# Performance work log

Measured on AMD Instinct MI355X. Metric: run time of the kernel, lower is better.

The kernel has to match this reference:

```python
import jax, jax.numpy as jnp
import numpy as np

LAMB = 0.01
DISTILL = 1.0
NUM_CLASSES = 10


def _reverse_seq(x, lens):
    # TF reverse_sequence semantics: reverse first `lens[i]` steps of row i.
    T = x.shape[1]
    t = jnp.arange(T)[None, :]
    idx = jnp.where(t < lens[:, None], lens[:, None] - 1 - t, t)
    return jnp.take_along_axis(x, idx[:, :, None], axis=1)


def _run_gru(x, lens, Wg, bg, Wc, bc):
    # TF GRUCell: r,z = sigmoid([x,h]Wg + bg); c = tanh([x, r*h]Wc + bc); h' = z*h + (1-z)*c
    # dynamic_rnn: past sequence_length, state is frozen and output is zero.
    N, T, _ = x.shape
    H = Wc.shape[1]
    h0 = jnp.zeros((N, H), x.dtype)

    def step(h, inp):
        x_t, t = inp
        xh = jnp.concatenate([x_t, h], axis=-1)
        rz = jax.nn.sigmoid(xh @ Wg + bg)
        r, z = jnp.split(rz, 2, axis=-1)
        c = jnp.tanh(jnp.concatenate([x_t, r * h], axis=-1) @ Wc + bc)
        h_new = z * h + (1.0 - z) * c
        valid = (t < lens)[:, None]
        return jnp.where(valid, h_new, h), jnp.where(valid, h_new, 0.0)

    _, outs = jax.lax.scan(step, h0, (x.transpose(1, 0, 2), jnp.arange(T)))
    return outs.transpose(1, 0, 2)  # [N, T, H]


def _bigru(x, lens, pfw, pbw):
    fw = _run_gru(x, lens, *pfw)
    bw = _reverse_seq(_run_gru(_reverse_seq(x, lens), lens, *pbw), lens)
    return jnp.concatenate([fw, bw], axis=-1)  # [N, T, 2H]


def _attention(out, Wa, ba, u):
    # additive attention: tanh projection -> score with context vector -> softmax -> weighted sum
    proj = jnp.tanh(out @ Wa + ba)                      # [N, T, A]
    score = jnp.squeeze(proj @ u, -1) / DISTILL         # [N, T]
    att = jax.nn.softmax(score, axis=1)
    vec = jnp.einsum('nt,nth->nh', att, out)            # [N, 2H]
    return vec, att


def setup_inputs() -> dict:
    key = jax.random.key(0)
    ks = jax.random.split(key, 40)
    B, D, S, E, H, C = 64, 40, 50, 200, 128, 10
    rn = lambda k, shp, s=0.1: (jax.random.normal(k, shp) * s).astype(jnp.float32)
    inp = {}
    inp['X_sentence'] = jax.random.normal(ks[0], (B, D, S, E), jnp.float32)
    inp['y'] = jax.random.randint(ks[1], (B,), 0, C).astype(jnp.int32)
    inp['sentence_length'] = jax.random.randint(ks[2], (B * D,), 1, S + 1).astype(jnp.int32)
    inp['document_length'] = jax.random.randint(ks[3], (B,), 1, D + 1).astype(jnp.int32)
    inp['dropout'] = 0
    inp['is_training'] = 0
    i = [4]
    def nxt():
        k = ks[i[0]]; i[0] += 1; return k
    for lvl, din in (('l', E), ('h', 2 * H)):
        for d in ('f', 'b'):
            inp['wg' + d + '_' + lvl] = rn(nxt(), (din + H, 2 * H))
            inp['bg' + d + '_' + lvl] = jnp.ones((2 * H,), jnp.float32)  # TF GRU gate bias init = 1.0
            inp['wc' + d + '_' + lvl] = rn(nxt(), (din + H, H))
            inp['bc' + d + '_' + lvl] = jnp.zeros((H,), jnp.float32)
        inp['wa_' + lvl] = rn(nxt(), (2 * H, H))
        inp['ba_' + lvl] = jnp.zeros((H,), jnp.float32)
    inp['uw'] = rn(nxt(), (H, 1), 1.0)  # random_normal stddev=1.0 as in source
    inp['us'] = rn(nxt(), (H, 1), 1.0)
    inp['wp'] = rn(nxt(), (2 * H, C))
    inp['bp'] = jnp.zeros((C,), jnp.float32)
    return inp


def reference(X_sentence, y, sentence_length, document_length, dropout, is_training,
              wgf_l, bgf_l, wcf_l, bcf_l, wgb_l, bgb_l, wcb_l, bcb_l, wa_l, ba_l,
              wgf_h, bgf_h, wcf_h, bcf_h, wgb_h, bgb_h, wcb_h, bcb_h, wa_h, ba_h,
              uw, us, wp, bp):
    # inference mode (is_training=False -> tf.layers.dropout is identity)
    B, D, S, E = X_sentence.shape
    x = X_sentence.reshape(B * D, S, E)
    # word level
    low = _bigru(x, sentence_length, (wgf_l, bgf_l, wcf_l, bcf_l), (wgb_l, bgb_l, wcb_l, bcb_l))
    sent_vec, att_low = _attention(low, wa_l, ba_l, uw)            # [B*D, 2H], [B*D, S]
    sent = sent_vec.reshape(B, D, -1)
    # sentence level
    high = _bigru(sent, document_length, (wgf_h, bgf_h, wcf_h, bcf_h), (wgb_h, bgb_h, wcb_h, bcb_h))
    doc_vec, att_high = _attention(high, wa_h, ba_h, us)           # [B, 2H], [B, D]
    logits = doc_vec @ wp + bp                                     # [B, C]
    logp = jax.nn.log_softmax(logits, axis=-1)
    loss = -jnp.mean(jnp.take_along_axis(logp, y[:, None], axis=1))
    # regularizer exactly as in source (note h kernel counted twice, h bias omitted)
    loss = loss + LAMB * (jnp.sum(wa_l ** 2) + jnp.sum(ba_l ** 2)
                          + 2.0 * jnp.sum(wa_h ** 2)
                          + jnp.sum(uw ** 2) + jnp.sum(us ** 2))
    predict = jnp.argmax(logits, axis=1).astype(jnp.int32)
    accuracy = jnp.mean((y == predict).astype(jnp.float32))
    return (loss, predict, accuracy, att_low, att_high)
```

## Files before the change

kernel.cpp:

```cpp
#include <hip/hip_runtime.h>
#include <hip/hip_bf16.h>


typedef __attribute__((ext_vector_type(8))) short short8;
typedef __attribute__((ext_vector_type(4))) float f32x4;

__device__ __forceinline__ float fsigmoid(float x) { return 1.f / (1.f + __expf(-x)); }
__device__ __forceinline__ float ftanh(float x)    { float e = __expf(2.f * x); return 1.f - 2.f / (e + 1.f); }

__device__ __forceinline__ unsigned short f2bf(float x) {
    unsigned int u = __builtin_bit_cast(unsigned int, x);
    u += 0x7fffu + ((u >> 16) & 1u);
    return (unsigned short)(u >> 16);
}
__device__ __forceinline__ float bf2f(unsigned short h) {
    unsigned int u = ((unsigned int)h) << 16;
    return __builtin_bit_cast(float, u);
}
__device__ __forceinline__ uint4 pack8(const unsigned short* v) {
    uint4 r;
    r.x = (unsigned int)v[0] | ((unsigned int)v[1] << 16);
    r.y = (unsigned int)v[2] | ((unsigned int)v[3] << 16);
    r.z = (unsigned int)v[4] | ((unsigned int)v[5] << 16);
    r.w = (unsigned int)v[6] | ((unsigned int)v[7] << 16);
    return r;
}
__device__ __forceinline__ void cvt8(const float* v, short8& hi, short8& lo) {
    unsigned short h[8], l[8];
#pragma unroll
    for (int j = 0; j < 8; ++j) {
        unsigned short hh = f2bf(v[j]);
        h[j] = hh;
        l[j] = f2bf(v[j] - bf2f(hh));
    }
    uint4 uh = pack8(h), ul = pack8(l);
    hi = __builtin_bit_cast(short8, uh);
    lo = __builtin_bit_cast(short8, ul);
}

__global__ __launch_bounds__(256) void pack_weights(
    const float* __restrict__ wg_f, const float* __restrict__ bg_f,
    const float* __restrict__ wc_f, const float* __restrict__ bc_f,
    const float* __restrict__ wg_b, const float* __restrict__ bg_b,
    const float* __restrict__ wc_b, const float* __restrict__ bc_b,
    float* __restrict__ W, float* __restrict__ bias, int E)
{
    int idx = blockIdx.x * 256 + threadIdx.x;
    if (idx < 768) {
        int c = idx; float v;
        if (c < 256) v = bg_f[c];
        else if (c < 384) v = bc_f[c - 256];
        else if (c < 640) v = bg_b[c - 384];
        else v = bc_b[c - 640];
        bias[c] = v;
    }
    if (idx >= E * 768) return;
    int k = idx / 768, c = idx - k * 768;
    float v;
    if (c < 256) v = wg_f[k * 256 + c];
    else if (c < 384) v = wc_f[k * 128 + (c - 256)];
    else if (c < 640) v = wg_b[k * 256 + (c - 384)];
    else v = wc_b[k * 128 + (c - 640)];
    W[idx] = v;
}

__global__ __launch_bounds__(256) void pack_a_frag(
    const float* __restrict__ src, uint4* __restrict__ dstH, uint4* __restrict__ dstL,
    int Mr16, int KC, int Ks)
{
    int idx = blockIdx.x * 256 + threadIdx.x;
    if (idx >= Mr16 * KC * 64) return;
    int lane = idx & 63;
    int g = idx >> 6;
    int mb = g / KC, kc = g - mb * KC;
    int m = lane & 15, quad = lane >> 4;
    int row = mb * 16 + m;
    int k0 = kc * 32 + quad * 8;
    const float* s = src + (size_t)row * Ks;
    unsigned short hi[8], lo[8];
#pragma unroll
    for (int j = 0; j < 8; ++j) {
        float x = (k0 + j < Ks) ? s[k0 + j] : 0.f;
        unsigned short h = f2bf(x);
        hi[j] = h;
        lo[j] = f2bf(x - bf2f(h));
    }
    dstH[idx] = pack8(hi);
    dstL[idx] = pack8(lo);
}

__global__ __launch_bounds__(256) void pack_w_frag(
    const float* __restrict__ src, uint4* __restrict__ dstH, uint4* __restrict__ dstL,
    int N16, int KC, int Ks, int N)
{
    int idx = blockIdx.x * 256 + threadIdx.x;
    if (idx >= N16 * KC * 64) return;
    int lane = idx & 63;
    int g = idx >> 6;
    int nb = g / KC, kc = g - nb * KC;
    int m = lane & 15, quad = lane >> 4;
    int n = nb * 16 + m;
    int k0 = kc * 32 + quad * 8;
    unsigned short hi[8], lo[8];
#pragma unroll
    for (int j = 0; j < 8; ++j) {
        float x = (k0 + j < Ks) ? src[(size_t)(k0 + j) * N + n] : 0.f;
        unsigned short h = f2bf(x);
        hi[j] = h;
        lo[j] = f2bf(x - bf2f(h));
    }
    dstH[idx] = pack8(hi);
    dstL[idx] = pack8(lo);
}

__global__ __launch_bounds__(256) void mfma_gemm(
    const uint4* __restrict__ Ah, const uint4* __restrict__ Al,
    const uint4* __restrict__ Bh, const uint4* __restrict__ Bl,
    const float* __restrict__ bias, float* __restrict__ C,
    int KC, int ldc, int act)
{
    int tid = threadIdx.x;
    int lane = tid & 63;
    int w = tid >> 6;
    int wm = w >> 1, wn = w & 1;
    int quad = lane >> 4, m = lane & 15;
    int bm = blockIdx.x, bn = blockIdx.y;
    f32x4 acc[4][4];
#pragma unroll
    for (int i = 0; i < 4; ++i)
#pragma unroll
        for (int j = 0; j < 4; ++j) acc[i][j] = (f32x4){0.f, 0.f, 0.f, 0.f};

    size_t aBase[4], bBase[4];
#pragma unroll
    for (int i = 0; i < 4; ++i) {
        aBase[i] = ((size_t)(bm * 8 + wm * 4 + i) * KC) * 64 + quad * 16 + m;
        bBase[i] = ((size_t)(bn * 8 + wn * 4 + i) * KC) * 64 + quad * 16 + m;
    }
    for (int kc = 0; kc < KC; ++kc) {
        short8 ah[4], al[4], bh[4], bl[4];
#pragma unroll
        for (int i = 0; i < 4; ++i) {
            ah[i] = __builtin_bit_cast(short8, Ah[aBase[i]]);
            al[i] = __builtin_bit_cast(short8, Al[aBase[i]]);
            bh[i] = __builtin_bit_cast(short8, Bh[bBase[i]]);
            bl[i] = __builtin_bit_cast(short8, Bl[bBase[i]]);
            aBase[i] += 64; bBase[i] += 64;
        }
#pragma unroll
        for (int i = 0; i < 4; ++i)
#pragma unroll
            for (int j = 0; j < 4; ++j) {
                acc[i][j] = __builtin_amdgcn_mfma_f32_16x16x32_bf16(ah[i], bh[j], acc[i][j], 0, 0, 0);
                acc[i][j] = __builtin_amdgcn_mfma_f32_16x16x32_bf16(ah[i], bl[j], acc[i][j], 0, 0, 0);
                acc[i][j] = __builtin_amdgcn_mfma_f32_16x16x32_bf16(al[i], bh[j], acc[i][j], 0, 0, 0);
            }
    }
#pragma unroll
    for (int i = 0; i < 4; ++i) {
        int row0 = bm * 128 + wm * 64 + i * 16 + quad * 4;
#pragma unroll
        for (int j = 0; j < 4; ++j) {
            int col = bn * 128 + wn * 64 + j * 16 + m;
            float b = bias[col];
#pragma unroll
            for (int r = 0; r < 4; ++r) {
                float v = acc[i][j][r] + b;
                if (act) v = ftanh(v);
                C[(size_t)(row0 + r) * ldc + col] = v;
            }
        }
    }
}

__global__ __launch_bounds__(256) void bigru_mfma(
    const float* __restrict__ G,
    const uint4* __restrict__ WgH, const uint4* __restrict__ WgL,
    const uint4* __restrict__ WcH, const uint4* __restrict__ WcL,
    const int* __restrict__ lens,
    float* __restrict__ outbuf,
    int rowOff, int T)
{
    __shared__ float hs[16][132];
    __shared__ float rs_[16][132];
    __shared__ float zs[16][132];
    __shared__ int Ls[16];

    int tid = threadIdx.x;
    int dir = blockIdx.x & 1;
    int rg0 = (blockIdx.x >> 1) * 16;
    int lane = tid & 63, w = tid >> 6;
    int quad = lane >> 4, mc = lane & 15;
    for (int i = tid; i < 16 * 132; i += 256) (&hs[0][0])[i] = 0.f;
    if (tid < 16) Ls[tid] = lens[rowOff + rg0 + tid];
    __syncthreads();
    const int goff = dir * 384;

    for (int t = 0; t < T; ++t) {
        int Lr[4], tir[4];
#pragma unroll
        for (int r = 0; r < 4; ++r) {
            int L = Ls[quad * 4 + r];
            Lr[r] = L;
            tir[r] = dir ? ((t < L) ? (L - 1 - t) : t) : t;
        }
        float gG[4][4], gC[2][4];
#pragma unroll
        for (int r = 0; r < 4; ++r) {
            const float* gbase = &G[((size_t)(rg0 + quad * 4 + r) * T + tir[r]) * 768 + goff];
#pragma unroll
            for (int i = 0; i < 4; ++i) gG[i][r] = gbase[(w * 4 + i) * 16 + mc];
#pragma unroll
            for (int i = 0; i < 2; ++i) gC[i][r] = gbase[256 + (w * 2 + i) * 16 + mc];
        }
        short8 ahh[4], ahl[4];
#pragma unroll
        for (int kc = 0; kc < 4; ++kc) {
            float v[8];
            const float* hp = &hs[mc][kc * 32 + quad * 8];
#pragma unroll
            for (int j = 0; j < 8; ++j) v[j] = hp[j];
            cvt8(v, ahh[kc], ahl[kc]);
        }
        f32x4 ga[4];
#pragma unroll
        for (int i = 0; i < 4; ++i) ga[i] = (f32x4){0.f, 0.f, 0.f, 0.f};
#pragma unroll
        for (int kc = 0; kc < 4; ++kc) {
#pragma unroll
            for (int i = 0; i < 4; ++i) {
                size_t idx = (((size_t)(dir * 16 + w * 4 + i) * 4 + kc) << 6) + lane;
                short8 bh = __builtin_bit_cast(short8, WgH[idx]);
                short8 bl = __builtin_bit_cast(short8, WgL[idx]);
                ga[i] = __builtin_amdgcn_mfma_f32_16x16x32_bf16(ahh[kc], bh, ga[i], 0, 0, 0);
                ga[i] = __builtin_amdgcn_mfma_f32_16x16x32_bf16(ahh[kc], bl, ga[i], 0, 0, 0);
                ga[i] = __builtin_amdgcn_mfma_f32_16x16x32_bf16(ahl[kc], bh, ga[i], 0, 0, 0);
            }
        }
#pragma unroll
        for (int i = 0; i < 4; ++i) {
            int n = (w * 4 + i) * 16 + mc;
#pragma unroll
            for (int r = 0; r < 4; ++r) {
                int m = quad * 4 + r;
                float s = fsigmoid(ga[i][r] + gG[i][r]);
                if (n < 128) rs_[m][n] = s * hs[m][n];
                else zs[m][n - 128] = s;
            }
        }
        __syncthreads();
        short8 arh[4], arl[4];
#pragma unroll
        for (int kc = 0; kc < 4; ++kc) {
            float v[8];
            const float* rp = &rs_[mc][kc * 32 + quad * 8];
#pragma unroll
            for (int j = 0; j < 8; ++j) v[j] = rp[j];
            cvt8(v, arh[kc], arl[kc]);
        }
        f32x4 ca[2];
#pragma unroll
        for (int i = 0; i < 2; ++i) ca[i] = (f32x4){0.f, 0.f, 0.f, 0.f};
#pragma unroll
        for (int kc = 0; kc < 4; ++kc) {
#pragma unroll
            for (int i = 0; i < 2; ++i) {
                size_t idx = (((size_t)(dir * 8 + w * 2 + i) * 4 + kc) << 6) + lane;
                short8 bh = __builtin_bit_cast(short8, WcH[idx]);
                short8 bl = __builtin_bit_cast(short8, WcL[idx]);
                ca[i] = __builtin_amdgcn_mfma_f32_16x16x32_bf16(arh[kc], bh, ca[i], 0, 0, 0);
                ca[i] = __builtin_amdgcn_mfma_f32_16x16x32_bf16(arh[kc], bl, ca[i], 0, 0, 0);
                ca[i] = __builtin_amdgcn_mfma_f32_16x16x32_bf16(arl[kc], bh, ca[i], 0, 0, 0);
            }
        }
#pragma unroll
        for (int i = 0; i < 2; ++i) {
            int n = (w * 2 + i) * 16 + mc;
#pragma unroll
            for (int r = 0; r < 4; ++r) {
                int m = quad * 4 + r;
                bool valid = (t < Lr[r]);
                float cd = ftanh(ca[i][r] + gC[i][r]);
                float z = zs[m][n];
                float h = hs[m][n];
                float hn = z * h + (1.f - z) * cd;
                float ov = valid ? hn : 0.f;
                if (valid) hs[m][n] = hn;
                outbuf[((size_t)(rg0 + m) * T + tir[r]) * 256 + dir * 128 + n] = ov;
            }
        }
        __syncthreads();
    }
}

__global__ __launch_bounds__(64) void attn_reduce(
    const float* __restrict__ proj, const float* __restrict__ outv,
    const float* __restrict__ u,
    float* __restrict__ att_out, float* __restrict__ vec,
    int T, int attRowOff)
{
    int n = blockIdx.x, lane = threadIdx.x;
    float s = 0.f;
    if (lane < T) {
        const float4* p = (const float4*)(proj + ((size_t)n * T + lane) * 128);
        const float4* uu = (const float4*)u;
        for (int k = 0; k < 32; ++k) {
            float4 a = p[k], b = uu[k];
            s += a.x * b.x + a.y * b.y + a.z * b.z + a.w * b.w;
        }
    }
    float m = (lane < T) ? s : -3.402823466e38f;
    for (int o = 32; o > 0; o >>= 1) m = fmaxf(m, __shfl_xor(m, o));
    float e = (lane < T) ? __expf(s - m) : 0.f;
    float sum = e;
    for (int o = 32; o > 0; o >>= 1) sum += __shfl_xor(sum, o);
    float att = e / sum;
    if (lane < T) att_out[(size_t)(attRowOff + n) * T + lane] = att;
    float4 acc = {0.f, 0.f, 0.f, 0.f};
    for (int t = 0; t < T; ++t) {
        float a = __shfl(att, t);
        float4 o4 = *(const float4*)&outv[((size_t)n * T + t) * 256 + lane * 4];
        acc.x += a * o4.x; acc.y += a * o4.y; acc.z += a * o4.z; acc.w += a * o4.w;
    }
    *(float4*)&vec[(size_t)n * 256 + lane * 4] = acc;
}

__global__ __launch_bounds__(256) void head_kernel(
    const float* __restrict__ dvec, const float* __restrict__ wp, const float* __restrict__ bp,
    const int* __restrict__ y,
    const float* __restrict__ wa_l, const float* __restrict__ ba_l, const float* __restrict__ wa_h,
    const float* __restrict__ uw, const float* __restrict__ us,
    float* __restrict__ out)
{
    __shared__ float lg[64][10];
    __shared__ float red[256];
    int tid = threadIdx.x;
    for (int idx = tid; idx < 640; idx += 256) {
        int r = idx / 10, c = idx % 10;
        float a = bp[c];
        const float* dv = dvec + r * 256;
        for (int k = 0; k < 256; ++k) a += dv[k] * wp[k * 10 + c];
        lg[r][c] = a;
    }
    __syncthreads();
    float lossv = 0.f, corr = 0.f;
    if (tid < 64) {
        float m = lg[tid][0]; int arg = 0;
        for (int c = 1; c < 10; ++c) if (lg[tid][c] > m) { m = lg[tid][c]; arg = c; }
        float se = 0.f;
        for (int c = 0; c < 10; ++c) se += __expf(lg[tid][c] - m);
        float lse = m + __logf(se);
        int yy = y[tid];
        lossv = -(lg[tid][yy] - lse);
        corr = (yy == arg) ? 1.f : 0.f;
        out[1 + tid] = (float)arg;
    }
    float rs = 0.f;
    for (int i = tid; i < 32768; i += 256) {
        float v = wa_l[i]; rs += v * v;
        float w = wa_h[i]; rs += 2.f * w * w;
    }
    if (tid < 128) {
        float v1 = ba_l[tid], v2 = uw[tid], v3 = us[tid];
        rs += v1 * v1 + v2 * v2 + v3 * v3;
    }
    red[tid] = lossv; __syncthreads();
    for (int o = 128; o > 0; o >>= 1) { if (tid < o) red[tid] += red[tid + o]; __syncthreads(); }
    float totLoss = red[0]; __syncthreads();
    red[tid] = corr; __syncthreads();
    for (int o = 128; o > 0; o >>= 1) { if (tid < o) red[tid] += red[tid + o]; __syncthreads(); }
    float totCorr = red[0]; __syncthreads();
    red[tid] = rs; __syncthreads();
    for (int o = 128; o > 0; o >>= 1) { if (tid < o) red[tid] += red[tid + o]; __syncthreads(); }
    float totReg = red[0];
    if (tid == 0) {
        out[0] = totLoss / 64.f + 0.01f * totReg;
        out[65] = totCorr / 64.f;
    }
}

extern "C" void kernel_launch(void* const* d_in, const int* in_sizes, int n_in,
                              void* d_out, int out_size, void* d_ws, size_t ws_size,
                              hipStream_t stream)
{
    const float* X    = (const float*)d_in[0];
    const int*   y    = (const int*)d_in[1];
    const int*   slen = (const int*)d_in[2];
    const int*   dlen = (const int*)d_in[3];
    const float* wgf_l = (const float*)d_in[6];
    const float* bgf_l = (const float*)d_in[7];
    const float* wcf_l = (const float*)d_in[8];
    const float* bcf_l = (const float*)d_in[9];
    const float* wgb_l = (const float*)d_in[10];
    const float* bgb_l = (const float*)d_in[11];
    const float* wcb_l = (const float*)d_in[12];
    const float* bcb_l = (const float*)d_in[13];
    const float* wa_l  = (const float*)d_in[14];
    const float* ba_l  = (const float*)d_in[15];
    const float* wgf_h = (const float*)d_in[16];
    const float* bgf_h = (const float*)d_in[17];
    const float* wcf_h = (const float*)d_in[18];
    const float* bcf_h = (const float*)d_in[19];
    const float* wgb_h = (const float*)d_in[20];
    const float* bgb_h = (const float*)d_in[21];
    const float* wcb_h = (const float*)d_in[22];
    const float* bcb_h = (const float*)d_in[23];
    const float* wa_h  = (const float*)d_in[24];
    const float* ba_h  = (const float*)d_in[25];
    const float* uw    = (const float*)d_in[26];
    const float* us    = (const float*)d_in[27];
    const float* wp    = (const float*)d_in[28];
    const float* bp    = (const float*)d_in[29];
    float* out = (float*)d_out;

    int NCH = 1;
    while (NCH < 8) {
        size_t M1t = 128000ull / NCH;
        size_t needB = (M1t * 1248ull + 6000000ull) * 4ull;
        if (needB <= ws_size) break;
        NCH *= 2;
    }
    size_t nRows = 2560 / NCH;
    size_t M1 = nRows * 50;

    float* G1     = (float*)d_ws;
    float* low    = G1 + M1 * 768;
    float* AXf    = low + M1 * 256;
    float* sent   = AXf + M1 * 224;
    float* Gs     = sent + 655360;
    float* high   = Gs + 1966080;
    float* projs  = high + 655360;
    float* dvec   = projs + 327680;
    float* pSf    = dvec + 16384;
    float* pHf    = pSf + 655360;
    float* WpackL = pHf + 655360;
    float* biasL  = WpackL + 153600;
    float* WLf    = biasL + 768;
    float* WpackH = WLf + 172032;
    float* biasH  = WpackH + 196608;
    float* WHf    = biasH + 768;
    float* WaLf   = WHf + 196608;
    float* WaHf   = WaLf + 32768;
    float* RgLf   = WaHf + 32768;
    float* RcLf   = RgLf + 65536;
    float* RgHf   = RcLf + 32768;
    float* RcHf   = RgHf + 65536;

    uint4* AXh = (uint4*)AXf;           uint4* AXl = (uint4*)(AXf + M1 * 112);
    uint4* ALh = (uint4*)G1;            uint4* ALl = (uint4*)(G1 + M1 * 128);
    float* proj = G1 + M1 * 256;
    uint4* pSh = (uint4*)pSf;           uint4* pSl = (uint4*)(pSf + 327680);
    uint4* pHh = (uint4*)pHf;           uint4* pHl = (uint4*)(pHf + 327680);
    uint4* WLh = (uint4*)WLf;           uint4* WLl = (uint4*)(WLf + 86016);
    uint4* WHh = (uint4*)WHf;           uint4* WHl = (uint4*)(WHf + 98304);
    uint4* WaLh = (uint4*)WaLf;         uint4* WaLl = (uint4*)(WaLf + 16384);
    uint4* WaHh = (uint4*)WaHf;         uint4* WaHl = (uint4*)(WaHf + 16384);
    uint4* RgLH = (uint4*)RgLf;         uint4* RgLL = (uint4*)(RgLf + 32768);
    uint4* RcLH = (uint4*)RcLf;         uint4* RcLL = (uint4*)(RcLf + 16384);
    uint4* RgHH = (uint4*)RgHf;         uint4* RgHL = (uint4*)(RgHf + 32768);
    uint4* RcHH = (uint4*)RcHf;         uint4* RcHL = (uint4*)(RcHf + 16384);

    pack_weights<<<600, 256, 0, stream>>>(wgf_l, bgf_l, wcf_l, bcf_l, wgb_l, bgb_l, wcb_l, bcb_l,
                                          WpackL, biasL, 200);
    pack_weights<<<768, 256, 0, stream>>>(wgf_h, bgf_h, wcf_h, bcf_h, wgb_h, bgb_h, wcb_h, bcb_h,
                                          WpackH, biasH, 256);
    pack_w_frag<<<84, 256, 0, stream>>>(WpackL, WLh, WLl, 48, 7, 200, 768);
    pack_w_frag<<<96, 256, 0, stream>>>(WpackH, WHh, WHl, 48, 8, 256, 768);
    pack_w_frag<<<16, 256, 0, stream>>>(wa_l, WaLh, WaLl, 8, 8, 256, 128);
    pack_w_frag<<<16, 256, 0, stream>>>(wa_h, WaHh, WaHl, 8, 8, 256, 128);
    pack_w_frag<<<16, 256, 0, stream>>>(wgf_l + 200 * 256, RgLH,        RgLL,        16, 4, 128, 256);
    pack_w_frag<<<16, 256, 0, stream>>>(wgb_l + 200 * 256, RgLH + 4096, RgLL + 4096, 16, 4, 128, 256);
    pack_w_frag<<< 8, 256, 0, stream>>>(wcf_l + 200 * 128, RcLH,        RcLL,         8, 4, 128, 128);
    pack_w_frag<<< 8, 256, 0, stream>>>(wcb_l + 200 * 128, RcLH + 2048, RcLL + 2048,  8, 4, 128, 128);
    pack_w_frag<<<16, 256, 0, stream>>>(wgf_h + 256 * 256, RgHH,        RgHL,        16, 4, 128, 256);
    pack_w_frag<<<16, 256, 0, stream>>>(wgb_h + 256 * 256, RgHH + 4096, RgHL + 4096, 16, 4, 128, 256);
    pack_w_frag<<< 8, 256, 0, stream>>>(wcf_h + 256 * 128, RcHH,        RcHL,         8, 4, 128, 128);
    pack_w_frag<<< 8, 256, 0, stream>>>(wcb_h + 256 * 128, RcHH + 2048, RcHL + 2048,  8, 4, 128, 128);

    for (int c = 0; c < NCH; ++c) {
        const float* Xc = X + (size_t)c * nRows * 50 * 200;
        int Mr16 = (int)(M1 / 16);
        pack_a_frag<<<(Mr16 * 7 * 64 + 255) / 256, 256, 0, stream>>>(Xc, AXh, AXl, Mr16, 7, 200);
        mfma_gemm<<<dim3((int)(M1 / 128), 6), 256, 0, stream>>>(AXh, AXl, WLh, WLl, biasL, G1, 7, 768, 0);
        bigru_mfma<<<(int)(nRows / 16) * 2, 256, 0, stream>>>(G1, RgLH, RgLL, RcLH, RcLL,
                                                              slen, low, (int)(c * nRows), 50);
        pack_a_frag<<<(Mr16 * 8 * 64 + 255) / 256, 256, 0, stream>>>(low, ALh, ALl, Mr16, 8, 256);
        mfma_gemm<<<dim3((int)(M1 / 128), 1), 256, 0, stream>>>(ALh, ALl, WaLh, WaLl, ba_l, proj, 8, 128, 1);
        attn_reduce<<<(int)nRows, 64, 0, stream>>>(proj, low, uw, out + 66, sent + (size_t)c * nRows * 256, 50, (int)(c * nRows));
    }
    pack_a_frag<<<(160 * 8 * 64 + 255) / 256, 256, 0, stream>>>(sent, pSh, pSl, 160, 8, 256);
    mfma_gemm<<<dim3(20, 6), 256, 0, stream>>>(pSh, pSl, WHh, WHl, biasH, Gs, 8, 768, 0);
    bigru_mfma<<<8, 256, 0, stream>>>(Gs, RgHH, RgHL, RcHH, RcHL, dlen, high, 0, 40);
    pack_a_frag<<<(160 * 8 * 64 + 255) / 256, 256, 0, stream>>>(high, pHh, pHl, 160, 8, 256);
    mfma_gemm<<<dim3(20, 1), 256, 0, stream>>>(pHh, pHl, WaHh, WaHl, ba_h, projs, 8, 128, 1);
    attn_reduce<<<64, 64, 0, stream>>>(projs, high, us, out + 128066, dvec, 40, 0);
    head_kernel<<<1, 256, 0, stream>>>(dvec, wp, bp, y, wa_l, ba_l, wa_h, uw, us, out);
}
```

Before: 1.341 ms.

## Fuse attention projection, scoring and pooling; keep GRU state in MFMA fragment layout

The separate pack_a_frag, tanh-projection GEMM and attn_reduce kernels are replaced by one attn_fused kernel per row. It stages the sequence in shared memory, runs the projection with MFMA, then does the score, softmax and weighted sum on chip. This removes the round trips for the projection and packed-fragment buffers. The bigru kernel now writes h and r*h straight into bf16 hi/lo fragment layout in shared memory, so the per-step split conversion is gone. The eight small recurrent-weight pack launches are merged into two. The fused attention kernel uses about 52 KB of shared memory per block, which may limit occupancy.

```diff
diff --git a/kernel.cpp b/kernel.cpp
--- a/kernel.cpp
+++ b/kernel.cpp
@@ -113,6 +113,38 @@
     dstL[idx] = pack8(lo);
 }
 
+__global__ __launch_bounds__(256) void pack_rec(
+    const float* __restrict__ wgf, const float* __restrict__ wgb,
+    const float* __restrict__ wcf, const float* __restrict__ wcb,
+    uint4* __restrict__ RgH, uint4* __restrict__ RgL,
+    uint4* __restrict__ RcH, uint4* __restrict__ RcL)
+{
+    int sel = blockIdx.y;
+    const float* src; uint4 *dH, *dL; int N16, N;
+    if (sel == 0)      { src = wgf; dH = RgH;        dL = RgL;        N16 = 16; N = 256; }
+    else if (sel == 1) { src = wgb; dH = RgH + 4096; dL = RgL + 4096; N16 = 16; N = 256; }
+    else if (sel == 2) { src = wcf; dH = RcH;        dL = RcL;        N16 = 8;  N = 128; }
+    else               { src = wcb; dH = RcH + 2048; dL = RcL + 2048; N16 = 8;  N = 128; }
+    int idx = blockIdx.x * 256 + threadIdx.x;
+    if (idx >= N16 * 4 * 64) return;
+    int lane = idx & 63;
+    int g = idx >> 6;
+    int nb = g / 4, kc = g - nb * 4;
+    int m = lane & 15, quad = lane >> 4;
+    int n = nb * 16 + m;
+    int k0 = kc * 32 + quad * 8;
+    unsigned short hi[8], lo[8];
+#pragma unroll
+    for (int j = 0; j < 8; ++j) {
+        float x = src[(size_t)(k0 + j) * N + n];
+        unsigned short h = f2bf(x);
+        hi[j] = h;
+        lo[j] = f2bf(x - bf2f(h));
+    }
+    dH[idx] = pack8(hi);
+    dL[idx] = pack8(lo);
+}
+
 __global__ __launch_bounds__(256) void mfma_gemm(
     const uint4* __restrict__ Ah, const uint4* __restrict__ Al,
     const uint4* __restrict__ Bh, const uint4* __restrict__ Bl,
@@ -182,8 +214,9 @@
     int rowOff, int T)
 {
     __shared__ float hs[16][132];
-    __shared__ float rs_[16][132];
     __shared__ float zs[16][132];
+    __shared__ uint4 hfH[4][64], hfL[4][64];
+    __shared__ uint4 rfH[4][64], rfL[4][64];
     __shared__ int Ls[16];
 
     int tid = threadIdx.x;
@@ -191,10 +224,15 @@
     int rg0 = (blockIdx.x >> 1) * 16;
     int lane = tid & 63, w = tid >> 6;
     int quad = lane >> 4, mc = lane & 15;
-    for (int i = tid; i < 16 * 132; i += 256) (&hs[0][0])[i] = 0.f;
+    for (int i = tid; i < 16 * 132; i += 256) { (&hs[0][0])[i] = 0.f; }
+    for (int i = tid; i < 256; i += 256) { hfH[0][i] = (uint4){0,0,0,0}; hfL[0][i] = (uint4){0,0,0,0}; }
     if (tid < 16) Ls[tid] = lens[rowOff + rg0 + tid];
     __syncthreads();
     const int goff = dir * 384;
+    unsigned short* hfHu = (unsigned short*)hfH;
+    unsigned short* hfLu = (unsigned short*)hfL;
+    unsigned short* rfHu = (unsigned short*)rfH;
+    unsigned short* rfLu = (unsigned short*)rfL;
 
     for (int t = 0; t < T; ++t) {
         int Lr[4], tir[4];
@@ -213,28 +251,21 @@
 #pragma unroll
             for (int i = 0; i < 2; ++i) gC[i][r] = gbase[256 + (w * 2 + i) * 16 + mc];
         }
-        short8 ahh[4], ahl[4];
+        f32x4 ga[4];
+#pragma unroll
+        for (int i = 0; i < 4; ++i) ga[i] = (f32x4){0.f, 0.f, 0.f, 0.f};
 #pragma unroll
         for (int kc = 0; kc < 4; ++kc) {
-            float v[8];
-            const float* hp = &hs[mc][kc * 32 + quad * 8];
-#pragma unroll
-            for (int j = 0; j < 8; ++j) v[j] = hp[j];
-            cvt8(v, ahh[kc], ahl[kc]);
-        }
-        f32x4 ga[4];
-#pragma unroll
-        for (int i = 0; i < 4; ++i) ga[i] = (f32x4){0.f, 0.f, 0.f, 0.f};
-#pragma unroll
-        for (int kc = 0; kc < 4; ++kc) {
+            short8 ah = __builtin_bit_cast(short8, hfH[kc][lane]);
+            short8 al = __builtin_bit_cast(short8, hfL[kc][lane]);
 #pragma unroll
             for (int i = 0; i < 4; ++i) {
                 size_t idx = (((size_t)(dir * 16 + w * 4 + i) * 4 + kc) << 6) + lane;
                 short8 bh = __builtin_bit_cast(short8, WgH[idx]);
                 short8 bl = __builtin_bit_cast(short8, WgL[idx]);
-                ga[i] = __builtin_amdgcn_mfma_f32_16x16x32_bf16(ahh[kc], bh, ga[i], 0, 0, 0);
-                ga[i] = __builtin_amdgcn_mfma_f32_16x16x32_bf16(ahh[kc], bl, ga[i], 0, 0, 0);
-                ga[i] = __builtin_amdgcn_mfma_f32_16x16x32_bf16(ahl[kc], bh, ga[i], 0, 0, 0);
+                ga[i] = __builtin_amdgcn_mfma_f32_16x16x32_bf16(ah, bh, ga[i], 0, 0, 0);
+                ga[i] = __builtin_amdgcn_mfma_f32_16x16x32_bf16(ah, bl, ga[i], 0, 0, 0);
+                ga[i] = __builtin_amdgcn_mfma_f32_16x16x32_bf16(al, bh, ga[i], 0, 0, 0);
             }
         }
 #pragma unroll
@@ -244,38 +275,39 @@
             for (int r = 0; r < 4; ++r) {
                 int m = quad * 4 + r;
                 float s = fsigmoid(ga[i][r] + gG[i][r]);
-                if (n < 128) rs_[m][n] = s * hs[m][n];
-                else zs[m][n - 128] = s;
+                if (n < 128) {
+                    float rh = s * hs[m][n];
+                    unsigned short hi = f2bf(rh);
+                    int fi = ((((n >> 5) * 64) + (((n >> 3) & 3) * 16) + m) << 3) + (n & 7);
+                    rfHu[fi] = hi;
+                    rfLu[fi] = f2bf(rh - bf2f(hi));
+                } else {
+                    zs[m][n - 128] = s;
+                }
             }
         }
         __syncthreads();
-        short8 arh[4], arl[4];
+        f32x4 ca[2];
+#pragma unroll
+        for (int i = 0; i < 2; ++i) ca[i] = (f32x4){0.f, 0.f, 0.f, 0.f};
 #pragma unroll
         for (int kc = 0; kc < 4; ++kc) {
-            float v[8];
-            const float* rp = &rs_[mc][kc * 32 + quad * 8];
-#pragma unroll
-            for (int j = 0; j < 8; ++j) v[j] = rp[j];
-            cvt8(v, arh[kc], arl[kc]);
-        }
-        f32x4 ca[2];
-#pragma unroll
-        for (int i = 0; i < 2; ++i) ca[i] = (f32x4){0.f, 0.f, 0.f, 0.f};
-#pragma unroll
-        for (int kc = 0; kc < 4; ++kc) {
+            short8 ar = __builtin_bit_cast(short8, rfH[kc][lane]);
+            short8 al = __builtin_bit_cast(short8, rfL[kc][lane]);
 #pragma unroll
             for (int i = 0; i < 2; ++i) {
                 size_t idx = (((size_t)(dir * 8 + w * 2 + i) * 4 + kc) << 6) + lane;
                 short8 bh = __builtin_bit_cast(short8, WcH[idx]);
                 short8 bl = __builtin_bit_cast(short8, WcL[idx]);
-                ca[i] = __builtin_amdgcn_mfma_f32_16x16x32_bf16(arh[kc], bh, ca[i], 0, 0, 0);
-                ca[i] = __builtin_amdgcn_mfma_f32_16x16x32_bf16(arh[kc], bl, ca[i], 0, 0, 0);
-                ca[i] = __builtin_amdgcn_mfma_f32_16x16x32_bf16(arl[kc], bh, ca[i], 0, 0, 0);
+                ca[i] = __builtin_amdgcn_mfma_f32_16x16x32_bf16(ar, bh, ca[i], 0, 0, 0);
+                ca[i] = __builtin_amdgcn_mfma_f32_16x16x32_bf16(ar, bl, ca[i], 0, 0, 0);
+                ca[i] = __builtin_amdgcn_mfma_f32_16x16x32_bf16(al, bh, ca[i], 0, 0, 0);
             }
         }
 #pragma unroll
         for (int i = 0; i < 2; ++i) {
             int n = (w * 2 + i) * 16 + mc;
+            int fi0 = ((((n >> 5) * 64) + (((n >> 3) & 3) * 16)) << 3) + (n & 7);
 #pragma unroll
             for (int r = 0; r < 4; ++r) {
                 int m = quad * 4 + r;
@@ -285,7 +317,13 @@
                 float h = hs[m][n];
                 float hn = z * h + (1.f - z) * cd;
                 float ov = valid ? hn : 0.f;
-                if (valid) hs[m][n] = hn;
+                if (valid) {
+                    hs[m][n] = hn;
+                    unsigned short hi = f2bf(hn);
+                    int fi = fi0 + (m << 3);
+                    hfHu[fi] = hi;
+                    hfLu[fi] = f2bf(hn - bf2f(hi));
+                }
                 outbuf[((size_t)(rg0 + m) * T + tir[r]) * 256 + dir * 128 + n] = ov;
             }
         }
@@ -293,36 +331,94 @@
     }
 }
 
-__global__ __launch_bounds__(64) void attn_reduce(
-    const float* __restrict__ proj, const float* __restrict__ outv,
-    const float* __restrict__ u,
-    float* __restrict__ att_out, float* __restrict__ vec,
+__global__ __launch_bounds__(256) void attn_fused(
+    const float* __restrict__ outv,
+    const uint4* __restrict__ WaH, const uint4* __restrict__ WaL,
+    const float* __restrict__ ba, const float* __restrict__ u,
+    float* __restrict__ att_out,
+    float* __restrict__ vec,
     int T, int attRowOff)
 {
-    int n = blockIdx.x, lane = threadIdx.x;
-    float s = 0.f;
-    if (lane < T) {
-        const float4* p = (const float4*)(proj + ((size_t)n * T + lane) * 128);
-        const float4* uu = (const float4*)u;
-        for (int k = 0; k < 32; ++k) {
-            float4 a = p[k], b = uu[k];
-            s += a.x * b.x + a.y * b.y + a.z * b.z + a.w * b.w;
-        }
-    }
-    float m = (lane < T) ? s : -3.402823466e38f;
-    for (int o = 32; o > 0; o >>= 1) m = fmaxf(m, __shfl_xor(m, o));
-    float e = (lane < T) ? __expf(s - m) : 0.f;
-    float sum = e;
-    for (int o = 32; o > 0; o >>= 1) sum += __shfl_xor(sum, o);
-    float att = e / sum;
-    if (lane < T) att_out[(size_t)(attRowOff + n) * T + lane] = att;
-    float4 acc = {0.f, 0.f, 0.f, 0.f};
-    for (int t = 0; t < T; ++t) {
-        float a = __shfl(att, t);
-        float4 o4 = *(const float4*)&outv[((size_t)n * T + t) * 256 + lane * 4];
-        acc.x += a * o4.x; acc.y += a * o4.y; acc.z += a * o4.z; acc.w += a * o4.w;
-    }
-    *(float4*)&vec[(size_t)n * 256 + lane * 4] = acc;
+    __shared__ float lowS[50][260];
+    __shared__ float scoreS[64];
+    __shared__ float attS[64];
+    int n = blockIdx.x;
+    int tid = threadIdx.x;
+    int lane = tid & 63, w = tid >> 6;
+    int quad = lane >> 4, mc = lane & 15;
+
+    const float4* src4 = (const float4*)(outv + (size_t)n * T * 256);
+    for (int idx = tid; idx < T * 64; idx += 256) {
+        int row = idx >> 6, c4 = idx & 63;
+        float4 v = src4[idx];
+        *(float4*)&lowS[row][c4 * 4] = v;
+    }
+    __syncthreads();
+
+    f32x4 acc[8];
+#pragma unroll
+    for (int j = 0; j < 8; ++j) acc[j] = (f32x4){0.f, 0.f, 0.f, 0.f};
+    int rowA = w * 16 + mc;
+    bool rowValid = rowA < T;
+#pragma unroll
+    for (int kc = 0; kc < 8; ++kc) {
+        float v[8];
+        if (rowValid) {
+            const float* p = &lowS[rowA][kc * 32 + quad * 8];
+#pragma unroll
+            for (int j = 0; j < 8; ++j) v[j] = p[j];
+        } else {
+#pragma unroll
+            for (int j = 0; j < 8; ++j) v[j] = 0.f;
+        }
+        short8 ah, al;
+        cvt8(v, ah, al);
+#pragma unroll
+        for (int nt = 0; nt < 8; ++nt) {
+            size_t idx = (((size_t)nt * 8 + kc) << 6) + lane;
+            short8 bh = __builtin_bit_cast(short8, WaH[idx]);
+            short8 bl = __builtin_bit_cast(short8, WaL[idx]);
+            acc[nt] = __builtin_amdgcn_mfma_f32_16x16x32_bf16(ah, bh, acc[nt], 0, 0, 0);
+            acc[nt] = __builtin_amdgcn_mfma_f32_16x16x32_bf16(ah, bl, acc[nt], 0, 0, 0);
+            acc[nt] = __builtin_amdgcn_mfma_f32_16x16x32_bf16(al, bh, acc[nt], 0, 0, 0);
+        }
+    }
+    float sc[4] = {0.f, 0.f, 0.f, 0.f};
+#pragma unroll
+    for (int nt = 0; nt < 8; ++nt) {
+        int col = nt * 16 + mc;
+        float bb = ba[col], uu = u[col];
+#pragma unroll
+        for (int r = 0; r < 4; ++r)
+            sc[r] += ftanh(acc[nt][r] + bb) * uu;
+    }
+#pragma unroll
+    for (int off = 1; off < 16; off <<= 1) {
+#pragma unroll
+        for (int r = 0; r < 4; ++r) sc[r] += __shfl_xor(sc[r], off);
+    }
+    if (mc == 0) {
+#pragma unroll
+        for (int r = 0; r < 4; ++r) scoreS[w * 16 + quad * 4 + r] = sc[r];
+    }
+    __syncthreads();
+    if (w == 0) {
+        float s = (lane < T) ? scoreS[lane] : -3.402823466e38f;
+        float m = s;
+#pragma unroll
+        for (int off = 1; off < 64; off <<= 1) m = fmaxf(m, __shfl_xor(m, off));
+        float e = (lane < T) ? __expf(s - m) : 0.f;
+        float sum = e;
+#pragma unroll
+        for (int off = 1; off < 64; off <<= 1) sum += __shfl_xor(sum, off);
+        float att = e / sum;
+        attS[lane] = att;
+        if (lane < T) att_out[(size_t)(attRowOff + n) * T + lane] = att;
+    }
+    __syncthreads();
+    float a = 0.f;
+    for (int t = 0; t < T; ++t) a += attS[t] * lowS[t][tid];
+    vec[(size_t)n * 256 + tid] = a;
 }
 
 __global__ __launch_bounds__(256) void head_kernel(
@@ -416,7 +512,7 @@
     int NCH = 1;
     while (NCH < 8) {
         size_t M1t = 128000ull / NCH;
-        size_t needB = (M1t * 1248ull + 6000000ull) * 4ull;
+        size_t needB = (M1t * 1248ull + 5200000ull) * 4ull;
         if (needB <= ws_size) break;
         NCH *= 2;
     }
@@ -429,11 +525,9 @@
     float* sent   = AXf + M1 * 224;
     float* Gs     = sent + 655360;
     float* high   = Gs + 1966080;
-    float* projs  = high + 655360;
-    float* dvec   = projs + 327680;
+    float* dvec   = high + 655360;
     float* pSf    = dvec + 16384;
-    float* pHf    = pSf + 655360;
-    float* WpackL = pHf + 655360;
+    float* WpackL = pSf + 655360;
     float* biasL  = WpackL + 153600;
     float* WLf    = biasL + 768;
     float* WpackH = WLf + 172032;
@@ -447,10 +541,7 @@
     float* RcHf   = RgHf + 65536;
 
     uint4* AXh = (uint4*)AXf;           uint4* AXl = (uint4*)(AXf + M1 * 112);
-    uint4* ALh = (uint4*)G1;            uint4* ALl = (uint4*)(G1 + M1 * 128);
-    float* proj = G1 + M1 * 256;
     uint4* pSh = (uint4*)pSf;           uint4* pSl = (uint4*)(pSf + 327680);
-    uint4* pHh = (uint4*)pHf;           uint4* pHl = (uint4*)(pHf + 327680);
     uint4* WLh = (uint4*)WLf;           uint4* WLl = (uint4*)(WLf + 86016);
     uint4* WHh = (uint4*)WHf;           uint4* WHl = (uint4*)(WHf + 98304);
     uint4* WaLh = (uint4*)WaLf;         uint4* WaLl = (uint4*)(WaLf + 16384);
@@ -468,14 +559,12 @@
     pack_w_frag<<<96, 256, 0, stream>>>(WpackH, WHh, WHl, 48, 8, 256, 768);
     pack_w_frag<<<16, 256, 0, stream>>>(wa_l, WaLh, WaLl, 8, 8, 256, 128);
     pack_w_frag<<<16, 256, 0, stream>>>(wa_h, WaHh, WaHl, 8, 8, 256, 128);
-    pack_w_frag<<<16, 256, 0, stream>>>(wgf_l + 200 * 256, RgLH,        RgLL,        16, 4, 128, 256);
-    pack_w_frag<<<16, 256, 0, stream>>>(wgb_l + 200 * 256, RgLH + 4096, RgLL + 4096, 16, 4, 128, 256);
-    pack_w_frag<<< 8, 256, 0, stream>>>(wcf_l + 200 * 128, RcLH,        RcLL,         8, 4, 128, 128);
-    pack_w_frag<<< 8, 256, 0, stream>>>(wcb_l + 200 * 128, RcLH + 2048, RcLL + 2048,  8, 4, 128, 128);
-    pack_w_frag<<<16, 256, 0, stream>>>(wgf_h + 256 * 256, RgHH,        RgHL,        16, 4, 128, 256);
-    pack_w_frag<<<16, 256, 0, stream>>>(wgb_h + 256 * 256, RgHH + 4096, RgHL + 4096, 16, 4, 128, 256);
-    pack_w_frag<<< 8, 256, 0, stream>>>(wcf_h + 256 * 128, RcHH,        RcHL,         8, 4, 128, 128);
-    pack_w_frag<<< 8, 256, 0, stream>>>(wcb_h + 256 * 128, RcHH + 2048, RcHL + 2048,  8, 4, 128, 128);
+    pack_rec<<<dim3(16, 4), 256, 0, stream>>>(wgf_l + 200 * 256, wgb_l + 200 * 256,
+                                              wcf_l + 200 * 128, wcb_l + 200 * 128,
+                                              RgLH, RgLL, RcLH, RcLL);
+    pack_rec<<<dim3(16, 4), 256, 0, stream>>>(wgf_h + 256 * 256, wgb_h + 256 * 256,
+                                              wcf_h + 256 * 128, wcb_h + 256 * 128,
+                                              RgHH, RgHL, RcHH, RcHL);
 
     for (int c = 0; c < NCH; ++c) {
         const float* Xc = X + (size_t)c * nRows * 50 * 200;
@@ -484,15 +573,12 @@
         mfma_gemm<<<dim3((int)(M1 / 128), 6), 256, 0, stream>>>(AXh, AXl, WLh, WLl, biasL, G1, 7, 768, 0);
         bigru_mfma<<<(int)(nRows / 16) * 2, 256, 0, stream>>>(G1, RgLH, RgLL, RcLH, RcLL,
                                                               slen, low, (int)(c * nRows), 50);
-        pack_a_frag<<<(Mr16 * 8 * 64 + 255) / 256, 256, 0, stream>>>(low, ALh, ALl, Mr16, 8, 256);
-        mfma_gemm<<<dim3((int)(M1 / 128), 1), 256, 0, stream>>>(ALh, ALl, WaLh, WaLl, ba_l, proj, 8, 128, 1);
-        attn_reduce<<<(int)nRows, 64, 0, stream>>>(proj, low, uw, out + 66, sent + (size_t)c * nRows * 256, 50, (int)(c * nRows));
+        attn_fused<<<(int)nRows, 256, 0, stream>>>(low, WaLh, WaLl, ba_l, uw,
+                                                   out + 66, sent + (size_t)c * nRows * 256, 50, (int)(c * nRows));
     }
     pack_a_frag<<<(160 * 8 * 64 + 255) / 256, 256, 0, stream>>>(sent, pSh, pSl, 160, 8, 256);
     mfma_gemm<<<dim3(20, 6), 256, 0, stream>>>(pSh, pSl, WHh, WHl, biasH, Gs, 8, 768, 0);
     bigru_mfma<<<8, 256, 0, stream>>>(Gs, RgHH, RgHL, RcHH, RcHL, dlen, high, 0, 40);
-    pack_a_frag<<<(160 * 8 * 64 + 255) / 256, 256, 0, stream>>>(high, pHh, pHl, 160, 8, 256);
-    mfma_gemm<<<dim3(20, 1), 256, 0, stream>>>(pHh, pHl, WaHh, WaHl, ba_h, projs, 8, 128, 1);
-    attn_reduce<<<64, 64, 0, stream>>>(projs, high, us, out + 128066, dvec, 40, 0);
+    attn_fused<<<64, 256, 0, stream>>>(high, WaHh, WaHl, ba_h, us, out + 128066, dvec, 40, 0);
     head_kernel<<<1, 256, 0, stream>>>(dvec, wp, bp, y, wa_l, ba_l, wa_h, uw, us, out);
 }
```

After: 1.237 ms. 7.8% less time.
